# Performance work log

Measured on AMD Instinct MI355X. Metric: run time of the kernel, lower is better.

Reference implementation:

```python
import jax, jax.numpy as jnp
import numpy as np

N = 50000
E = 500000
CH = 256
H1, C1 = 4, 64
H2, C2 = 8, 32
CONCAT = H1 * C1 + H2 * C2  # 512


def setup_inputs() -> dict:
    key = jax.random.key(0)
    ks = jax.random.split(key, 16)
    s = 0.05
    x = jax.random.normal(ks[0], (N, CH), dtype=jnp.float32)
    edge_index = jax.random.randint(ks[1], (2, E), 0, N, dtype=jnp.int64)
    return {
        "x": x,
        "edge_index": edge_index,
        "gamma": jnp.ones((CH,), jnp.float32),
        "beta": jnp.zeros((CH,), jnp.float32),
        "W1": jax.random.normal(ks[2], (CH, H1 * C1), jnp.float32) * s,
        "a_src1": jax.random.normal(ks[3], (H1, C1), jnp.float32) * s,
        "a_dst1": jax.random.normal(ks[4], (H1, C1), jnp.float32) * s,
        "b1": jnp.zeros((H1 * C1,), jnp.float32),
        "W2": jax.random.normal(ks[5], (CH, H2 * C2), jnp.float32) * s,
        "a_src2": jax.random.normal(ks[6], (H2, C2), jnp.float32) * s,
        "a_dst2": jax.random.normal(ks[7], (H2, C2), jnp.float32) * s,
        "b2": jnp.zeros((H2 * C2,), jnp.float32),
        "Wu": jax.random.normal(ks[8], (CONCAT, CH), jnp.float32) * s,
        "bu": jnp.zeros((CH,), jnp.float32),
    }


def _layer_norm(x, gamma, beta, eps=1e-5):
    mu = jnp.mean(x, axis=-1, keepdims=True)
    var = jnp.var(x, axis=-1, keepdims=True)
    return (x - mu) * jax.lax.rsqrt(var + eps) * gamma + beta


def _gat_conv(x, src, dst, W, a_src, a_dst, bias, heads, out_ch, n_nodes):
    # x: [N, CH] -> per-head projection h: [N, H, C]
    h = (x @ W).reshape(n_nodes, heads, out_ch)
    alpha_s = jnp.einsum('nhc,hc->nh', h, a_src)  # [N, H]
    alpha_d = jnp.einsum('nhc,hc->nh', h, a_dst)  # [N, H]
    e = jax.nn.leaky_relu(alpha_s[src] + alpha_d[dst], negative_slope=0.2)  # [E, H]
    # segment softmax over incoming edges of each dst node (self-loops guarantee nonempty segments)
    m = jax.ops.segment_max(e, dst, num_segments=n_nodes)
    ex = jnp.exp(e - m[dst])
    denom = jax.ops.segment_sum(ex, dst, num_segments=n_nodes)
    a = ex / (denom[dst] + 1e-16)  # [E, H]
    msg = h[src] * a[:, :, None]  # [E, H, C]
    out = jax.ops.segment_sum(msg, dst, num_segments=n_nodes)  # [N, H, C]
    return out.reshape(n_nodes, heads * out_ch) + bias


def reference(x, edge_index, gamma, beta, W1, a_src1, a_dst1, b1,
              W2, a_src2, a_dst2, b2, Wu, bu):
    n = x.shape[0]
    # add self-loops (PyG GATConv default)
    loop = jnp.arange(n, dtype=edge_index.dtype)
    src = jnp.concatenate([edge_index[0], loop])
    dst = jnp.concatenate([edge_index[1], loop])

    residual = x
    x_norm = _layer_norm(x, gamma, beta)
    out1 = _gat_conv(x_norm, src, dst, W1, a_src1, a_dst1, b1, H1, C1, n)
    out2 = _gat_conv(x_norm, src, dst, W2, a_src2, a_dst2, b2, H2, C2, n)
    x_cat = jax.nn.elu(jnp.concatenate([out1, out2], axis=-1))
    unified = x_cat @ Wu + bu
    return residual + unified
```

## Files before the change

kernel.cpp:

```cpp
#include <hip/hip_runtime.h>
#include <hip/hip_bf16.h>
#include <math.h>

constexpr int CH = 256;
constexpr int CC = 512;
constexpr int AP = 16;

typedef __bf16 bf16x8 __attribute__((ext_vector_type(8)));
typedef float  f32x4  __attribute__((ext_vector_type(4)));
typedef float  f32x2  __attribute__((ext_vector_type(2)));
typedef int    i32x4  __attribute__((ext_vector_type(4)));
typedef __attribute__((address_space(3))) void lds_void;
typedef __attribute__((address_space(1))) void glb_void;

__device__ inline unsigned short f2bf(float f) {
    union { float f; unsigned u; } v; v.f = f;
    unsigned r = v.u + 0x7FFFu + ((v.u >> 16) & 1u);
    return (unsigned short)(r >> 16);
}

__global__ void fused_pre_kernel(const float* __restrict__ x, const float* __restrict__ gamma,
                                 const float* __restrict__ beta,
                                 const float* __restrict__ W1, const float* __restrict__ W2,
                                 const float* __restrict__ Wu,
                                 const float* __restrict__ as1, const float* __restrict__ ad1,
                                 const float* __restrict__ as2, const float* __restrict__ ad2,
                                 unsigned short* __restrict__ xnb,
                                 unsigned short* __restrict__ WT1, unsigned short* __restrict__ WTu,
                                 unsigned short* __restrict__ Pt,
                                 const int* __restrict__ dstE, int* __restrict__ deg,
                                 int N, int E, int LNB) {
    int b = blockIdx.x;
    int t = threadIdx.x;
    if (b < LNB) {
        int wid = b * 4 + (t >> 6);
        int lane = t & 63;
        if (wid >= N) return;
        const float4 v = *(const float4*)(x + (size_t)wid * CH + lane * 4);
        float s = v.x + v.y + v.z + v.w;
        float sq = v.x * v.x + v.y * v.y + v.z * v.z + v.w * v.w;
        #pragma unroll
        for (int o = 32; o; o >>= 1) { s += __shfl_xor(s, o); sq += __shfl_xor(sq, o); }
        float mu = s * (1.0f / CH);
        float var = sq * (1.0f / CH) - mu * mu;
        float rs = rsqrtf(var + 1e-5f);
        float4 g = *(const float4*)(gamma + lane * 4);
        float4 bb = *(const float4*)(beta + lane * 4);
        unsigned short o0 = f2bf((v.x - mu) * rs * g.x + bb.x);
        unsigned short o1 = f2bf((v.y - mu) * rs * g.y + bb.y);
        unsigned short o2 = f2bf((v.z - mu) * rs * g.z + bb.z);
        unsigned short o3 = f2bf((v.w - mu) * rs * g.w + bb.w);
        uint2 pk;
        pk.x = (unsigned)o0 | ((unsigned)o1 << 16);
        pk.y = (unsigned)o2 | ((unsigned)o3 << 16);
        *(uint2*)(xnb + (size_t)wid * CH + lane * 4) = pk;
    } else if (b < LNB + 512) {
        int idx = (b - LNB) * 256 + t;
        int n = idx >> 8, k = idx & 255;
        float v = (n < 256) ? W1[(size_t)k * 256 + n] : W2[(size_t)k * 256 + (n - 256)];
        WT1[idx] = f2bf(v);
    } else if (b < LNB + 1024) {
        int idx = (b - LNB - 512) * 256 + t;
        int n = idx >> 9, k = idx & 511;
        WTu[idx] = f2bf(Wu[(size_t)k * 256 + n]);
    } else if (b < LNB + 1056) {
        int n = b - LNB - 1024;
        int k = t;
        float a = 0.f;
        if (n < 4) {
            for (int c = 0; c < 64; ++c) a += W1[(size_t)k * 256 + n * 64 + c] * as1[n * 64 + c];
        } else if (n < 12) {
            for (int c = 0; c < 32; ++c) a += W2[(size_t)k * 256 + (n - 4) * 32 + c] * as2[(n - 4) * 32 + c];
        } else if (n >= 16 && n < 20) {
            for (int c = 0; c < 64; ++c) a += W1[(size_t)k * 256 + (n - 16) * 64 + c] * ad1[(n - 16) * 64 + c];
        } else if (n >= 20 && n < 28) {
            for (int c = 0; c < 32; ++c) a += W2[(size_t)k * 256 + (n - 20) * 32 + c] * ad2[(n - 20) * 32 + c];
        }
        Pt[n * 256 + k] = f2bf(a);
    } else {
        int i = (b - LNB - 1056) * 256 + t;
        if (i < E) atomicAdd(&deg[dstE[i]], 1);
    }
}

template<int K>
__device__ inline void gemm_core32(const unsigned short* __restrict__ Ab,
                                   const unsigned short* __restrict__ Bt,
                                   unsigned short* As, unsigned short* Bs,
                                   f32x4 acc[4][4], int m0, int n0, int M) {
    const int t = threadIdx.x;
    const int lane = t & 63;
    const int wave = t >> 6;
    const int wr = wave >> 1, wc = wave & 1;
    const int rowc = lane >> 2;
    const int eslot = lane & 3;
    const int fr = lane & 15;
    const int fkb = (lane >> 4) << 4;

    auto stage = [&](int buf, int k0) {
        #pragma unroll
        for (int c = 0; c < 2; ++c) {
            int chunk = wave * 2 + c;
            int row = chunk * 16 + rowc;
            int se = ((eslot ^ (row & 3)) << 3);
            int gra = m0 + row; if (gra >= M) gra = M - 1;
            __builtin_amdgcn_global_load_lds((const glb_void*)(Ab + (size_t)gra * K + k0 + se),
                                             (lds_void*)&As[buf * 4096 + chunk * 512], 16, 0, 0);
            __builtin_amdgcn_global_load_lds((const glb_void*)(Bt + (size_t)(n0 + row) * K + k0 + se),
                                             (lds_void*)&Bs[buf * 4096 + chunk * 512], 16, 0, 0);
        }
    };
    auto compute = [&](int buf) {
        const int bb = buf * 8192;
        bf16x8 af[4], bfr[4];
        #pragma unroll
        for (int m = 0; m < 4; ++m) {
            int r = wr * 64 + m * 16 + fr;
            int pc = fkb ^ ((r & 3) << 4);
            af[m] = *(const bf16x8*)((const char*)As + bb + r * 64 + pc);
        }
        #pragma unroll
        for (int n = 0; n < 4; ++n) {
            int r = wc * 64 + n * 16 + fr;
            int pc = fkb ^ ((r & 3) << 4);
            bfr[n] = *(const bf16x8*)((const char*)Bs + bb + r * 64 + pc);
        }
        #pragma unroll
        for (int m = 0; m < 4; ++m)
            #pragma unroll
            for (int n = 0; n < 4; ++n)
                acc[m][n] = __builtin_amdgcn_mfma_f32_16x16x32_bf16(af[m], bfr[n], acc[m][n], 0, 0, 0);
    };

    stage(0, 0);
    __syncthreads();
    int cur = 0;
    #pragma unroll
    for (int k0 = 32; k0 < K; k0 += 32) {
        stage(cur ^ 1, k0);
        compute(cur);
        __syncthreads();
        cur ^= 1;
    }
    compute(cur);
}

__global__ __launch_bounds__(256) void gemm1_mfma(
    const unsigned short* __restrict__ Ab, const unsigned short* __restrict__ Bt,
    const unsigned short* __restrict__ Pt,
    unsigned char* __restrict__ Hq,
    float* __restrict__ alpha_src, float* __restrict__ alpha_dst, int M, int MB, int G1B) {
    __shared__ unsigned short As[8192];
    __shared__ unsigned short Bs[8192];
    const int s = blockIdx.x;
    const int lane = threadIdx.x & 63;
    const int wave = threadIdx.x >> 6;
    const int fr = lane & 15;
    const int fkb = (lane >> 4) << 4;
    const int orow = (lane >> 4) * 4;

    if (s < G1B) {
        const int xcd = s & 7;
        const int jj = s >> 3;
        const int n_blk = jj & 3;
        const int m_blk = (jj >> 2) * 8 + xcd;
        if (m_blk >= MB) return;
        const int m0 = m_blk * 128, n0 = n_blk * 128;
        const int wr = wave >> 1, wc = wave & 1;
        f32x4 acc[4][4] = {};
        gemm_core32<256>(Ab, Bt, As, Bs, acc, m0, n0, M);
        #pragma unroll
        for (int m = 0; m < 4; ++m)
            #pragma unroll
            for (int j = 0; j < 4; ++j) {
                int r = m0 + wr * 64 + m * 16 + orow + j;
                if (r < M) {
                    #pragma unroll
                    for (int n = 0; n < 4; ++n) {
                        int ccol = n0 + wc * 64 + n * 16 + fr;
                        unsigned q = (unsigned)__builtin_amdgcn_cvt_pk_fp8_f32(
                            acc[m][n][j], acc[m][n][j], 0, false) & 0xffu;
                        Hq[(size_t)r * CC + ccol] = (unsigned char)q;
                    }
                }
            }
        return;
    }
    const int m_blk = s - G1B;
    if (m_blk >= MB) return;
    const int m0 = m_blk * 128;
    {
        int rr_in = lane >> 5;
        int e32 = lane & 31;
        #pragma unroll
        for (int c = 0; c < 4; ++c) {
            int chunk = wave * 4 + c;
            int rr = chunk * 2 + rr_in;
            const unsigned short* g = Pt + rr * 256 + ((e32 ^ (rr & 7)) << 3);
            __builtin_amdgcn_global_load_lds((const glb_void*)g,
                                             (lds_void*)&Bs[chunk * 512], 16, 0, 0);
        }
    }
    const int rowc = lane >> 2, eslot = lane & 3;
    auto stageA = [&](int buf, int k0) {
        #pragma unroll
        for (int c = 0; c < 2; ++c) {
            int chunk = wave * 2 + c;
            int row = chunk * 16 + rowc;
            int gra = m0 + row; if (gra >= M) gra = M - 1;
            const unsigned short* g = Ab + (size_t)gra * 256 + k0 + ((eslot ^ (row & 3)) << 3);
            __builtin_amdgcn_global_load_lds((const glb_void*)g,
                                             (lds_void*)&As[buf * 4096 + chunk * 512], 16, 0, 0);
        }
    };
    f32x4 a2[2][2] = {};
    auto computeA = [&](int buf, int k0) {
        const int bb = buf * 8192;
        bf16x8 af[2], bf_[2];
        #pragma unroll
        for (int m = 0; m < 2; ++m) {
            int r = wave * 32 + m * 16 + fr;
            int pc = fkb ^ ((r & 3) << 4);
            af[m] = *(const bf16x8*)((const char*)As + bb + r * 64 + pc);
        }
        #pragma unroll
        for (int n = 0; n < 2; ++n) {
            int rb = n * 16 + fr;
            int pcb = (k0 * 2 + fkb) ^ ((rb & 7) << 4);
            bf_[n] = *(const bf16x8*)((const char*)Bs + rb * 512 + pcb);
        }
        #pragma unroll
        for (int m = 0; m < 2; ++m)
            #pragma unroll
            for (int n = 0; n < 2; ++n)
                a2[m][n] = __builtin_amdgcn_mfma_f32_16x16x32_bf16(af[m], bf_[n], a2[m][n], 0, 0, 0);
    };
    stageA(0, 0);
    __syncthreads();
    int cur = 0;
    #pragma unroll
    for (int k0 = 32; k0 < 256; k0 += 32) {
        stageA(cur ^ 1, k0);
        computeA(cur, k0 - 32);
        __syncthreads();
        cur ^= 1;
    }
    computeA(cur, 224);
    #pragma unroll
    for (int m = 0; m < 2; ++m)
        #pragma unroll
        for (int j = 0; j < 4; ++j) {
            int r = m0 + wave * 32 + m * 16 + orow + j;
            if (fr < 12 && r < M) {
                alpha_src[(size_t)r * AP + fr] = a2[m][0][j];
                alpha_dst[(size_t)r * AP + fr] = a2[m][1][j];
            }
        }
}

__global__ __launch_bounds__(256) void gemm2_mfma(const unsigned short* __restrict__ Ab,
                                                  const unsigned short* __restrict__ Bt,
                                                  const float* __restrict__ bu,
                                                  const float* __restrict__ xres,
                                                  float* __restrict__ C, int M, int MB) {
    __shared__ unsigned short As[8192];
    __shared__ unsigned short Bs[8192];
    const int s = blockIdx.x;
    const int xcd = s & 7;
    const int jj = s >> 3;
    const int n_blk = jj & 1;
    const int m_blk = (jj >> 1) * 8 + xcd;
    if (m_blk >= MB) return;
    const int m0 = m_blk * 128, n0 = n_blk * 128;
    const int lane = threadIdx.x & 63;
    const int wave = threadIdx.x >> 6;
    const int wr = wave >> 1, wc = wave & 1;
    f32x4 acc[4][4] = {};
    gemm_core32<512>(Ab, Bt, As, Bs, acc, m0, n0, M);
    const int fr = lane & 15;
    const int orow = (lane >> 4) * 4;
    #pragma unroll
    for (int m = 0; m < 4; ++m)
        #pragma unroll
        for (int j = 0; j < 4; ++j) {
            int r = m0 + wr * 64 + m * 16 + orow + j;
            if (r < M) {
                #pragma unroll
                for (int n = 0; n < 4; ++n) {
                    int ccol = n0 + wc * 64 + n * 16 + fr;
                    float xr = __builtin_nontemporal_load(&xres[(size_t)r * CH + ccol]);
                    __builtin_nontemporal_store(acc[m][n][j] + bu[ccol] + xr,
                                                &C[(size_t)r * CH + ccol]);
                }
            }
        }
}

__global__ __launch_bounds__(256) void scan1_kernel(const int* __restrict__ deg, int* __restrict__ pre,
                                                    int* __restrict__ bsum, int n) {
    __shared__ int wsum[4];
    int t = threadIdx.x, lane = t & 63, w = t >> 6;
    int base = blockIdx.x * 1024 + t * 4;
    int v0 = base     < n ? deg[base]     + 1 : 0;
    int v1 = base + 1 < n ? deg[base + 1] + 1 : 0;
    int v2 = base + 2 < n ? deg[base + 2] + 1 : 0;
    int v3 = base + 3 < n ? deg[base + 3] + 1 : 0;
    int s = v0 + v1 + v2 + v3;
    int sc = s;
    #pragma unroll
    for (int o = 1; o < 64; o <<= 1) { int xx = __shfl_up(sc, o); if (lane >= o) sc += xx; }
    if (lane == 63) wsum[w] = sc;
    __syncthreads();
    int wo = 0;
    #pragma unroll
    for (int k = 0; k < 4; ++k) if (k < w) wo += wsum[k];
    int p = wo + sc - s;
    if (base     < n) pre[base]     = p; p += v0;
    if (base + 1 < n) pre[base + 1] = p; p += v1;
    if (base + 2 < n) pre[base + 2] = p; p += v2;
    if (base + 3 < n) pre[base + 3] = p;
    if (t == 255) bsum[blockIdx.x] = wo + sc;
}
__global__ void scan2_kernel(int* __restrict__ bsum, int nb) {
    int lane = threadIdx.x;
    int v = lane < nb ? bsum[lane] : 0;
    int sc = v;
    #pragma unroll
    for (int o = 1; o < 64; o <<= 1) { int xx = __shfl_up(sc, o); if (lane >= o) sc += xx; }
    if (lane < nb) bsum[lane] = sc - v;
}
__global__ void scan3_csr_kernel(const int* __restrict__ pre, const int* __restrict__ bsum,
                                 int* __restrict__ offsets, int* __restrict__ cursor,
                                 int* __restrict__ csr, int n, int total) {
    int i = blockIdx.x * 256 + threadIdx.x;
    if (i < n) {
        int off = pre[i] + bsum[i >> 10];
        offsets[i] = off;
        cursor[i] = off + 1;
        csr[off] = i;
    }
    if (i == 0) offsets[n] = total;
}
__global__ void scatter_kernel(const int* __restrict__ src, const int* __restrict__ dst,
                               int* __restrict__ cursor, int* __restrict__ csr, int E) {
    int i = blockIdx.x * blockDim.x + threadIdx.x;
    if (i < E) {
        int pos = atomicAdd(&cursor[dst[i]], 1);
        csr[pos] = src[i];
    }
}

__global__ void aggregate_kernel(const unsigned char* __restrict__ Hq,
                                 const float* __restrict__ alpha_src,
                                 const float* __restrict__ alpha_dst,
                                 const int* __restrict__ offsets,
                                 const int* __restrict__ csr,
                                 const float* __restrict__ b1, const float* __restrict__ b2,
                                 unsigned short* __restrict__ xcb, int N) {
    int n = __builtin_amdgcn_readfirstlane((int)((blockIdx.x * blockDim.x + threadIdx.x) >> 6));
    int lane = threadIdx.x & 63;
    if (n >= N) return;
    int beg = offsets[n], end = offsets[n + 1];
    int c0 = lane * 8;
    int hid = (lane < 32) ? (lane >> 3) : (4 + ((lane - 32) >> 2));
    float adh = alpha_dst[(size_t)n * AP + hid];

    float ssum = 0.f;
    f32x2 A0 = {0.f, 0.f}, A1 = {0.f, 0.f}, A2 = {0.f, 0.f}, A3 = {0.f, 0.f};

    int i = beg;
    for (; i + 4 <= end; i += 4) {
        int ss[4];
        #pragma unroll
        for (int u = 0; u < 4; ++u) ss[u] = csr[i + u];
        float lw[4];
        #pragma unroll
        for (int u = 0; u < 4; ++u) lw[u] = alpha_src[(size_t)ss[u] * AP + hid];
        uint2 hv[4];
        #pragma unroll
        for (int u = 0; u < 4; ++u) hv[u] = *(const uint2*)(Hq + (size_t)ss[u] * CC + c0);
        #pragma unroll
        for (int u = 0; u < 4; ++u) {
            float l = lw[u] + adh;
            l = fmaxf(l, 0.2f * l);
            float wv = __expf(l);
            ssum += wv;
            f32x2 wv2; wv2[0] = wv; wv2[1] = wv;
            A0 += __builtin_amdgcn_cvt_pk_f32_fp8(hv[u].x, false) * wv2;
            A1 += __builtin_amdgcn_cvt_pk_f32_fp8(hv[u].x, true)  * wv2;
            A2 += __builtin_amdgcn_cvt_pk_f32_fp8(hv[u].y, false) * wv2;
            A3 += __builtin_amdgcn_cvt_pk_f32_fp8(hv[u].y, true)  * wv2;
        }
    }
    for (; i < end; ++i) {
        int s0 = csr[i];
        float l = alpha_src[(size_t)s0 * AP + hid] + adh;
        uint2 hv0 = *(const uint2*)(Hq + (size_t)s0 * CC + c0);
        l = fmaxf(l, 0.2f * l);
        float wv = __expf(l);
        ssum += wv;
        f32x2 wv2; wv2[0] = wv; wv2[1] = wv;
        A0 += __builtin_amdgcn_cvt_pk_f32_fp8(hv0.x, false) * wv2;
        A1 += __builtin_amdgcn_cvt_pk_f32_fp8(hv0.x, true)  * wv2;
        A2 += __builtin_amdgcn_cvt_pk_f32_fp8(hv0.y, false) * wv2;
        A3 += __builtin_amdgcn_cvt_pk_f32_fp8(hv0.y, true)  * wv2;
    }

    float inv = 1.0f / (ssum + 1e-16f);
    const float* bb = (c0 < 256) ? (b1 + c0) : (b2 + (c0 - 256));
    float4 bb0 = *(const float4*)(bb), bb1 = *(const float4*)(bb + 4);
    float o[8];
    o[0] = A0[0] * inv + bb0.x; o[1] = A0[1] * inv + bb0.y;
    o[2] = A1[0] * inv + bb0.z; o[3] = A1[1] * inv + bb0.w;
    o[4] = A2[0] * inv + bb1.x; o[5] = A2[1] * inv + bb1.y;
    o[6] = A3[0] * inv + bb1.z; o[7] = A3[1] * inv + bb1.w;
    #pragma unroll
    for (int j = 0; j < 8; ++j) o[j] = o[j] > 0.f ? o[j] : expm1f(o[j]);
    unsigned short u[8];
    #pragma unroll
    for (int j = 0; j < 8; ++j) u[j] = f2bf(o[j]);
    i32x4 pk;
    pk[0] = (int)((unsigned)u[0] | ((unsigned)u[1] << 16));
    pk[1] = (int)((unsigned)u[2] | ((unsigned)u[3] << 16));
    pk[2] = (int)((unsigned)u[4] | ((unsigned)u[5] << 16));
    pk[3] = (int)((unsigned)u[6] | ((unsigned)u[7] << 16));
    __builtin_nontemporal_store(pk, (i32x4*)(xcb + (size_t)n * CC + c0));
}

extern "C" void kernel_launch(void* const* d_in, const int* in_sizes, int n_in,
                              void* d_out, int out_size, void* d_ws, size_t ws_size,
                              hipStream_t stream) {
    const float* x     = (const float*)d_in[0];
    const int*   ei    = (const int*)d_in[1];
    const float* gamma = (const float*)d_in[2];
    const float* beta  = (const float*)d_in[3];
    const float* W1    = (const float*)d_in[4];
    const float* as1   = (const float*)d_in[5];
    const float* ad1   = (const float*)d_in[6];
    const float* b1    = (const float*)d_in[7];
    const float* W2    = (const float*)d_in[8];
    const float* as2   = (const float*)d_in[9];
    const float* ad2   = (const float*)d_in[10];
    const float* b2    = (const float*)d_in[11];
    const float* Wu    = (const float*)d_in[12];
    const float* bu    = (const float*)d_in[13];
    float* out = (float*)d_out;

    const int N = in_sizes[0] / CH;
    const int E = in_sizes[1] / 2;
    const int* src = ei;
    const int* dst = ei + E;

    char* w = (char*)d_ws;
    auto alloc = [&](size_t bytes) { char* p = w; w += (bytes + 255) & ~(size_t)255; return p; };
    unsigned char*  Hq  = (unsigned char*)alloc((size_t)N * CC);
    unsigned short* xnb = (unsigned short*)alloc((size_t)N * CH * 2);
    unsigned short* xcb = (unsigned short*)alloc((size_t)N * CC * 2);
    unsigned short* WT1 = (unsigned short*)alloc(512 * 256 * 2);
    unsigned short* WTu = (unsigned short*)alloc(256 * 512 * 2);
    unsigned short* Pt  = (unsigned short*)alloc(32 * 256 * 2);
    float* alpha_src = (float*)alloc((size_t)N * AP * 4);
    float* alpha_dst = (float*)alloc((size_t)N * AP * 4);
    int* deg     = (int*)alloc((size_t)N * 4);
    int* pre     = (int*)alloc((size_t)N * 4);
    int* bsum    = (int*)alloc(64 * 4);
    int* offsets = (int*)alloc(((size_t)N + 1) * 4);
    int* cursor  = (int*)alloc((size_t)N * 4);
    int* csr     = (int*)alloc(((size_t)E + N) * 4);

    hipMemsetAsync(deg, 0, (size_t)N * 4, stream);

    const int LNB = (N + 3) / 4;
    const int HB = (E + 255) / 256;
    fused_pre_kernel<<<LNB + 1056 + HB, 256, 0, stream>>>(
        x, gamma, beta, W1, W2, Wu, as1, ad1, as2, ad2,
        xnb, WT1, WTu, Pt, dst, deg, N, E, LNB);

    const int MB = (N + 127) / 128;
    const int MB8 = ((MB + 7) / 8) * 8;
    const int G1B = MB8 * 4;
    gemm1_mfma<<<G1B + MB, 256, 0, stream>>>(xnb, WT1, Pt, Hq, alpha_src, alpha_dst, N, MB, G1B);

    int nb = (N + 1023) / 1024;
    scan1_kernel<<<nb, 256, 0, stream>>>(deg, pre, bsum, N);
    scan2_kernel<<<1, 64, 0, stream>>>(bsum, nb);
    scan3_csr_kernel<<<(N + 255) / 256, 256, 0, stream>>>(pre, bsum, offsets, cursor, csr, N, E + N);
    scatter_kernel<<<(E + 255) / 256, 256, 0, stream>>>(src, dst, cursor, csr, E);

    aggregate_kernel<<<(N + 3) / 4, 256, 0, stream>>>(Hq, alpha_src, alpha_dst, offsets, csr,
                                                      b1, b2, xcb, N);

    gemm2_mfma<<<MB8 * 2, 256, 0, stream>>>(xcb, WTu, bu, x, out, N, MB);
}
```

Measured before the change: 204.4 us.

## Split aggregation across two waves per node and move degree count into GEMM1

The aggregation kernel now gives each destination node two waves (128 threads), with each lane covering 4 fp8 channels instead of 8. This raises parallelism and memory-level concurrency for the gather, at the cost of duplicated index, alpha and exp work per edge. Separately, the degree-histogram atomics move from the pre-processing kernel into extra trailing blocks of the GEMM1 launch, so they overlap with the matmul instead of with layer norm.

Result: no change. 206.0 us (+0.8%).

```diff
diff --git a/kernel.cpp b/kernel.cpp
--- a/kernel.cpp
+++ b/kernel.cpp
@@ -9,7 +9,7 @@
 typedef __bf16 bf16x8 __attribute__((ext_vector_type(8)));
 typedef float  f32x4  __attribute__((ext_vector_type(4)));
 typedef float  f32x2  __attribute__((ext_vector_type(2)));
-typedef int    i32x4  __attribute__((ext_vector_type(4)));
+typedef int    i32x2  __attribute__((ext_vector_type(2)));
 typedef __attribute__((address_space(3))) void lds_void;
 typedef __attribute__((address_space(1))) void glb_void;
 
@@ -28,8 +28,7 @@
                                  unsigned short* __restrict__ xnb,
                                  unsigned short* __restrict__ WT1, unsigned short* __restrict__ WTu,
                                  unsigned short* __restrict__ Pt,
-                                 const int* __restrict__ dstE, int* __restrict__ deg,
-                                 int N, int E, int LNB) {
+                                 int N, int LNB) {
     int b = blockIdx.x;
     int t = threadIdx.x;
     if (b < LNB) {
@@ -63,7 +62,7 @@
         int idx = (b - LNB - 512) * 256 + t;
         int n = idx >> 9, k = idx & 511;
         WTu[idx] = f2bf(Wu[(size_t)k * 256 + n]);
-    } else if (b < LNB + 1056) {
+    } else {
         int n = b - LNB - 1024;
         int k = t;
         float a = 0.f;
@@ -77,9 +76,6 @@
             for (int c = 0; c < 32; ++c) a += W2[(size_t)k * 256 + (n - 20) * 32 + c] * ad2[(n - 20) * 32 + c];
         }
         Pt[n * 256 + k] = f2bf(a);
-    } else {
-        int i = (b - LNB - 1056) * 256 + t;
-        if (i < E) atomicAdd(&deg[dstE[i]], 1);
     }
 }
 
@@ -149,10 +145,16 @@
     const unsigned short* __restrict__ Ab, const unsigned short* __restrict__ Bt,
     const unsigned short* __restrict__ Pt,
     unsigned char* __restrict__ Hq,
-    float* __restrict__ alpha_src, float* __restrict__ alpha_dst, int M, int MB, int G1B) {
+    float* __restrict__ alpha_src, float* __restrict__ alpha_dst, int M, int MB, int G1B,
+    const int* __restrict__ dstE, int* __restrict__ deg, int E) {
     __shared__ unsigned short As[8192];
     __shared__ unsigned short Bs[8192];
     const int s = blockIdx.x;
+    if (s >= G1B + MB) {
+        int i = (s - G1B - MB) * 256 + threadIdx.x;
+        if (i < E) atomicAdd(&deg[dstE[i]], 1);
+        return;
+    }
     const int lane = threadIdx.x & 63;
     const int wave = threadIdx.x >> 6;
     const int fr = lane & 15;
@@ -357,16 +359,18 @@
                                  const int* __restrict__ csr,
                                  const float* __restrict__ b1, const float* __restrict__ b2,
                                  unsigned short* __restrict__ xcb, int N) {
-    int n = __builtin_amdgcn_readfirstlane((int)((blockIdx.x * blockDim.x + threadIdx.x) >> 6));
-    int lane = threadIdx.x & 63;
+    int t = threadIdx.x;
+    int n = __builtin_amdgcn_readfirstlane((int)(blockIdx.x * 2 + (t >> 7)));
     if (n >= N) return;
+    int lane = t & 63;
+    int half = (t >> 6) & 1;
+    int c0 = half * 256 + lane * 4;
+    int hid = (c0 < 256) ? (c0 >> 6) : (4 + ((c0 - 256) >> 5));
     int beg = offsets[n], end = offsets[n + 1];
-    int c0 = lane * 8;
-    int hid = (lane < 32) ? (lane >> 3) : (4 + ((lane - 32) >> 2));
     float adh = alpha_dst[(size_t)n * AP + hid];
 
     float ssum = 0.f;
-    f32x2 A0 = {0.f, 0.f}, A1 = {0.f, 0.f}, A2 = {0.f, 0.f}, A3 = {0.f, 0.f};
+    f32x2 A0 = {0.f, 0.f}, A1 = {0.f, 0.f};
 
     int i = beg;
     for (; i + 4 <= end; i += 4) {
@@ -376,9 +380,9 @@
         float lw[4];
         #pragma unroll
         for (int u = 0; u < 4; ++u) lw[u] = alpha_src[(size_t)ss[u] * AP + hid];
-        uint2 hv[4];
-        #pragma unroll
-        for (int u = 0; u < 4; ++u) hv[u] = *(const uint2*)(Hq + (size_t)ss[u] * CC + c0);
+        unsigned hv[4];
+        #pragma unroll
+        for (int u = 0; u < 4; ++u) hv[u] = *(const unsigned*)(Hq + (size_t)ss[u] * CC + c0);
         #pragma unroll
         for (int u = 0; u < 4; ++u) {
             float l = lw[u] + adh;
@@ -386,45 +390,37 @@
             float wv = __expf(l);
             ssum += wv;
             f32x2 wv2; wv2[0] = wv; wv2[1] = wv;
-            A0 += __builtin_amdgcn_cvt_pk_f32_fp8(hv[u].x, false) * wv2;
-            A1 += __builtin_amdgcn_cvt_pk_f32_fp8(hv[u].x, true)  * wv2;
-            A2 += __builtin_amdgcn_cvt_pk_f32_fp8(hv[u].y, false) * wv2;
-            A3 += __builtin_amdgcn_cvt_pk_f32_fp8(hv[u].y, true)  * wv2;
+            A0 += __builtin_amdgcn_cvt_pk_f32_fp8(hv[u], false) * wv2;
+            A1 += __builtin_amdgcn_cvt_pk_f32_fp8(hv[u], true)  * wv2;
         }
     }
     for (; i < end; ++i) {
         int s0 = csr[i];
         float l = alpha_src[(size_t)s0 * AP + hid] + adh;
-        uint2 hv0 = *(const uint2*)(Hq + (size_t)s0 * CC + c0);
+        unsigned hv0 = *(const unsigned*)(Hq + (size_t)s0 * CC + c0);
         l = fmaxf(l, 0.2f * l);
         float wv = __expf(l);
         ssum += wv;
         f32x2 wv2; wv2[0] = wv; wv2[1] = wv;
-        A0 += __builtin_amdgcn_cvt_pk_f32_fp8(hv0.x, false) * wv2;
-        A1 += __builtin_amdgcn_cvt_pk_f32_fp8(hv0.x, true)  * wv2;
-        A2 += __builtin_amdgcn_cvt_pk_f32_fp8(hv0.y, false) * wv2;
-        A3 += __builtin_amdgcn_cvt_pk_f32_fp8(hv0.y, true)  * wv2;
+        A0 += __builtin_amdgcn_cvt_pk_f32_fp8(hv0, false) * wv2;
+        A1 += __builtin_amdgcn_cvt_pk_f32_fp8(hv0, true)  * wv2;
     }
 
     float inv = 1.0f / (ssum + 1e-16f);
     const float* bb = (c0 < 256) ? (b1 + c0) : (b2 + (c0 - 256));
-    float4 bb0 = *(const float4*)(bb), bb1 = *(const float4*)(bb + 4);
-    float o[8];
-    o[0] = A0[0] * inv + bb0.x; o[1] = A0[1] * inv + bb0.y;
-    o[2] = A1[0] * inv + bb0.z; o[3] = A1[1] * inv + bb0.w;
-    o[4] = A2[0] * inv + bb1.x; o[5] = A2[1] * inv + bb1.y;
-    o[6] = A3[0] * inv + bb1.z; o[7] = A3[1] * inv + bb1.w;
-    #pragma unroll
-    for (int j = 0; j < 8; ++j) o[j] = o[j] > 0.f ? o[j] : expm1f(o[j]);
-    unsigned short u[8];
-    #pragma unroll
-    for (int j = 0; j < 8; ++j) u[j] = f2bf(o[j]);
-    i32x4 pk;
+    float4 bb4 = *(const float4*)(bb);
+    float o[4];
+    o[0] = A0[0] * inv + bb4.x; o[1] = A0[1] * inv + bb4.y;
+    o[2] = A1[0] * inv + bb4.z; o[3] = A1[1] * inv + bb4.w;
+    #pragma unroll
+    for (int j = 0; j < 4; ++j) o[j] = o[j] > 0.f ? o[j] : expm1f(o[j]);
+    unsigned short u[4];
+    #pragma unroll
+    for (int j = 0; j < 4; ++j) u[j] = f2bf(o[j]);
+    i32x2 pk;
     pk[0] = (int)((unsigned)u[0] | ((unsigned)u[1] << 16));
     pk[1] = (int)((unsigned)u[2] | ((unsigned)u[3] << 16));
-    pk[2] = (int)((unsigned)u[4] | ((unsigned)u[5] << 16));
-    pk[3] = (int)((unsigned)u[6] | ((unsigned)u[7] << 16));
-    __builtin_nontemporal_store(pk, (i32x4*)(xcb + (size_t)n * CC + c0));
+    __builtin_nontemporal_store(pk, (i32x2*)(xcb + (size_t)n * CC + c0));
 }
 
 extern "C" void kernel_launch(void* const* d_in, const int* in_sizes, int n_in,
@@ -471,15 +467,16 @@
     hipMemsetAsync(deg, 0, (size_t)N * 4, stream);
 
     const int LNB = (N + 3) / 4;
-    const int HB = (E + 255) / 256;
-    fused_pre_kernel<<<LNB + 1056 + HB, 256, 0, stream>>>(
+    fused_pre_kernel<<<LNB + 1056, 256, 0, stream>>>(
         x, gamma, beta, W1, W2, Wu, as1, ad1, as2, ad2,
-        xnb, WT1, WTu, Pt, dst, deg, N, E, LNB);
+        xnb, WT1, WTu, Pt, N, LNB);
 
     const int MB = (N + 127) / 128;
     const int MB8 = ((MB + 7) / 8) * 8;
     const int G1B = MB8 * 4;
-    gemm1_mfma<<<G1B + MB, 256, 0, stream>>>(xnb, WT1, Pt, Hq, alpha_src, alpha_dst, N, MB, G1B);
+    const int HB = (E + 255) / 256;
+    gemm1_mfma<<<G1B + MB + HB, 256, 0, stream>>>(xnb, WT1, Pt, Hq, alpha_src, alpha_dst,
+                                                  N, MB, G1B, dst, deg, E);
 
     int nb = (N + 1023) / 1024;
     scan1_kernel<<<nb, 256, 0, stream>>>(deg, pre, bsum, N);
@@ -487,7 +484,7 @@
     scan3_csr_kernel<<<(N + 255) / 256, 256, 0, stream>>>(pre, bsum, offsets, cursor, csr, N, E + N);
     scatter_kernel<<<(E + 255) / 256, 256, 0, stream>>>(src, dst, cursor, csr, E);
 
-    aggregate_kernel<<<(N + 3) / 4, 256, 0, stream>>>(Hq, alpha_src, alpha_dst, offsets, csr,
+    aggregate_kernel<<<(N + 1) / 2, 256, 0, stream>>>(Hq, alpha_src, alpha_dst, offsets, csr,
                                                       b1, b2, xcb, N);
 
     gemm2_mfma<<<MB8 * 2, 256, 0, stream>>>(xcb, WTu, bu, x, out, N, MB);
```

## Drop memset and scan2 launches by folding work into neighbouring kernels

Applied to the files above, without the earlier changes.

Degree zeroing moves from a separate memset into extra blocks of the pre kernel, and the degree histogram atomics move into extra blocks of the first GEMM launch. The single-block scan2 kernel is removed; scan3 instead sums preceding block totals with a short serial loop per thread. This cuts two launches and their serialization gaps, at the cost of redundant bsum reads in scan3 and atomics now sharing the GEMM launch.

After: 194.3 us. 1.05x faster.

```diff
diff --git a/kernel.cpp b/kernel.cpp
--- a/kernel.cpp
+++ b/kernel.cpp
@@ -28,8 +28,8 @@
                                  unsigned short* __restrict__ xnb,
                                  unsigned short* __restrict__ WT1, unsigned short* __restrict__ WTu,
                                  unsigned short* __restrict__ Pt,
-                                 const int* __restrict__ dstE, int* __restrict__ deg,
-                                 int N, int E, int LNB) {
+                                 int* __restrict__ deg,
+                                 int N, int LNB) {
     int b = blockIdx.x;
     int t = threadIdx.x;
     if (b < LNB) {
@@ -79,7 +79,7 @@
         Pt[n * 256 + k] = f2bf(a);
     } else {
         int i = (b - LNB - 1056) * 256 + t;
-        if (i < E) atomicAdd(&deg[dstE[i]], 1);
+        if (i < N) deg[i] = 0;
     }
 }
 
@@ -149,10 +149,16 @@
     const unsigned short* __restrict__ Ab, const unsigned short* __restrict__ Bt,
     const unsigned short* __restrict__ Pt,
     unsigned char* __restrict__ Hq,
-    float* __restrict__ alpha_src, float* __restrict__ alpha_dst, int M, int MB, int G1B) {
+    float* __restrict__ alpha_src, float* __restrict__ alpha_dst, int M, int MB, int G1B,
+    const int* __restrict__ dstE, int* __restrict__ deg, int E) {
     __shared__ unsigned short As[8192];
     __shared__ unsigned short Bs[8192];
     const int s = blockIdx.x;
+    if (s >= G1B + MB) {
+        int i = (s - G1B - MB) * 256 + threadIdx.x;
+        if (i < E) atomicAdd(&deg[dstE[i]], 1);
+        return;
+    }
     const int lane = threadIdx.x & 63;
     const int wave = threadIdx.x >> 6;
     const int fr = lane & 15;
@@ -321,20 +327,15 @@
     if (base + 3 < n) pre[base + 3] = p;
     if (t == 255) bsum[blockIdx.x] = wo + sc;
 }
-__global__ void scan2_kernel(int* __restrict__ bsum, int nb) {
-    int lane = threadIdx.x;
-    int v = lane < nb ? bsum[lane] : 0;
-    int sc = v;
-    #pragma unroll
-    for (int o = 1; o < 64; o <<= 1) { int xx = __shfl_up(sc, o); if (lane >= o) sc += xx; }
-    if (lane < nb) bsum[lane] = sc - v;
-}
 __global__ void scan3_csr_kernel(const int* __restrict__ pre, const int* __restrict__ bsum,
                                  int* __restrict__ offsets, int* __restrict__ cursor,
                                  int* __restrict__ csr, int n, int total) {
     int i = blockIdx.x * 256 + threadIdx.x;
     if (i < n) {
-        int off = pre[i] + bsum[i >> 10];
+        int chunk = i >> 10;
+        int boff = 0;
+        for (int k = 0; k < chunk; ++k) boff += bsum[k];
+        int off = pre[i] + boff;
         offsets[i] = off;
         cursor[i] = off + 1;
         csr[off] = i;
@@ -468,22 +469,21 @@
     int* cursor  = (int*)alloc((size_t)N * 4);
     int* csr     = (int*)alloc(((size_t)E + N) * 4);
 
-    hipMemsetAsync(deg, 0, (size_t)N * 4, stream);
-
     const int LNB = (N + 3) / 4;
-    const int HB = (E + 255) / 256;
-    fused_pre_kernel<<<LNB + 1056 + HB, 256, 0, stream>>>(
+    const int DEGZ = (N + 255) / 256;
+    fused_pre_kernel<<<LNB + 1056 + DEGZ, 256, 0, stream>>>(
         x, gamma, beta, W1, W2, Wu, as1, ad1, as2, ad2,
-        xnb, WT1, WTu, Pt, dst, deg, N, E, LNB);
+        xnb, WT1, WTu, Pt, deg, N, LNB);
 
     const int MB = (N + 127) / 128;
     const int MB8 = ((MB + 7) / 8) * 8;
     const int G1B = MB8 * 4;
-    gemm1_mfma<<<G1B + MB, 256, 0, stream>>>(xnb, WT1, Pt, Hq, alpha_src, alpha_dst, N, MB, G1B);
+    const int HB = (E + 255) / 256;
+    gemm1_mfma<<<G1B + MB + HB, 256, 0, stream>>>(xnb, WT1, Pt, Hq, alpha_src, alpha_dst,
+                                                  N, MB, G1B, dst, deg, E);
 
     int nb = (N + 1023) / 1024;
     scan1_kernel<<<nb, 256, 0, stream>>>(deg, pre, bsum, N);
-    scan2_kernel<<<1, 64, 0, stream>>>(bsum, nb);
     scan3_csr_kernel<<<(N + 255) / 256, 256, 0, stream>>>(pre, bsum, offsets, cursor, csr, N, E + N);
     scatter_kernel<<<(E + 255) / 256, 256, 0, stream>>>(src, dst, cursor, csr, E);
 
```
